# Optimization experiments

Measured on AMD Instinct MI355X. Metric: run time of the kernel, lower is better.

Reference implementation:

```python
import jax, jax.numpy as jnp
import numpy as np
import math

DILATION_RATES = (1, 2, 4, 8)


def setup_inputs() -> dict:
    key = jax.random.key(0)
    B, S, D = 2, 2048, 512
    R = len(DILATION_RATES)
    ks = jax.random.split(key, 8)
    s = 0.02  # init scale
    x = jax.random.normal(ks[0], (B, S, D), dtype=jnp.float32)
    Wq = jax.random.normal(ks[1], (D, D), dtype=jnp.float32) * s
    Wk = jax.random.normal(ks[2], (D, D), dtype=jnp.float32) * s
    Wv = jax.random.normal(ks[3], (D, D), dtype=jnp.float32) * s
    Wr = jax.random.normal(ks[4], (R, D, D), dtype=jnp.float32) * s  # per-rate projections
    Wo = jax.random.normal(ks[5], (R * D, D), dtype=jnp.float32) * s
    bq = jnp.zeros((D,), jnp.float32)
    bk = jnp.zeros((D,), jnp.float32)
    bv = jnp.zeros((D,), jnp.float32)
    br = jnp.zeros((R, D), jnp.float32)
    bo = jnp.zeros((D,), jnp.float32)
    return {"x": x, "Wq": Wq, "bq": bq, "Wk": Wk, "bk": bk, "Wv": Wv, "bv": bv,
            "Wr": Wr, "br": br, "Wo": Wo, "bo": bo}


def reference(x, Wq, bq, Wk, bk, Wv, bv, Wr, br, Wo, bo):
    B, S, D = x.shape
    Q = x @ Wq + bq
    K = x @ Wk + bk
    V = x @ Wv + bv
    # Dense scores are identical across rates in the original (recomputed each loop);
    # compute once for the same math.
    scores = jnp.einsum('bid,bjd->bij', Q, K) / math.sqrt(D)  # [B,S,S]
    idx = jnp.arange(S)
    outs, attns = [], []
    for r, rate in enumerate(DILATION_RATES):
        # mask[i, j] = 1 iff (j % rate == 0) and (j <= i)
        mask = (idx[None, :] % rate == 0) & (idx[None, :] <= idx[:, None])  # [S,S]
        sc = jnp.where(mask[None, :, :], scores, jnp.float32(-1e9))
        attn = jax.nn.softmax(sc, axis=-1)  # dropout is identity at eval
        attns.append(attn)
        ctx = jnp.einsum('bij,bjd->bid', attn, V)
        outs.append(ctx @ Wr[r] + br[r])
    combined = jnp.concatenate(outs, axis=-1)  # [B,S,4D]
    output = combined @ Wo + bo  # [B,S,D]
    avg_attention = jnp.mean(jnp.stack(attns, axis=0), axis=0)  # [B,S,S]
    return output, avg_attention
```

## Files before the change

### kernel.cpp

```cpp
#include <hip/hip_runtime.h>
#include <hip/hip_bf16.h>
#include <math.h>

#define B_ 2
#define S_ 2048
#define D_ 512
#define R_ 4
#define KP 3840

typedef __attribute__((ext_vector_type(8))) __bf16 bf16x8;
typedef __attribute__((ext_vector_type(4))) float f32x4;

enum { M_QKV = 0, M_SCORES = 1, M_WEFFT = 2, M_W2T = 3, M_PF = 4 };

__device__ __forceinline__ void g2l16(const void* gp, void* lp) {
    __builtin_amdgcn_global_load_lds(
        (const __attribute__((address_space(1))) unsigned int*)(unsigned long long)gp,
        (__attribute__((address_space(3))) unsigned int*)(unsigned int)(unsigned long long)lp,
        16, 0, 0);
}

template<int MODE, int TBM, int TBN>
__global__ __launch_bounds__(256) void mfma_nt(
    const short* __restrict__ A, const short* __restrict__ B,
    const float* __restrict__ bias, void* __restrict__ Cv,
    int lda, int ldb, int ldc, int K,
    long strA, long strB, long strC, long strBias, float scale)
{
    constexpr int WM = TBM / 2, WN = TBN / 2;
    constexpr int FM = WM / 16, FN = WN / 16;

    __shared__ __bf16 sAt[TBM * 64];
    __shared__ __bf16 sBt[TBN * 64];

    const int tid  = threadIdx.x;
    const int lane = tid & 63, wid = tid >> 6;
    const int ln15 = lane & 15, quad = lane >> 4;
    const int wy = wid & 1, wx = wid >> 1;

    const int by   = (MODE == M_PF) ? (gridDim.y - 1 - blockIdx.y) : blockIdx.y;
    const int col0 = blockIdx.x * TBN;
    const int row0 = by * TBM;
    const int z    = blockIdx.z;

    if constexpr (MODE == M_SCORES) {
        if (col0 > row0 + TBM - 1) return;
    }

    const short* Ab = A + (size_t)z * strA;
    const short* Bb = B + (size_t)z * strB;
    const float* biasb = bias + (size_t)z * strBias;

    int rate = 1, seg = 0;
    if constexpr (MODE == M_W2T) {
        int rIdx;
        if      (col0 >= 3584) { rate = 8; seg = 3584; rIdx = 3; }
        else if (col0 >= 3072) { rate = 4; seg = 3072; rIdx = 2; }
        else if (col0 >= 2048) { rate = 2; seg = 2048; rIdx = 1; }
        else                   { rate = 1; seg = 0;    rIdx = 0; }
        Ab += (size_t)rIdx * D_ * D_;
    }

    f32x4 acc[FM][FN];
    #pragma unroll
    for (int u = 0; u < FM; ++u)
        #pragma unroll
        for (int v = 0; v < FN; ++v)
            acc[u][v] = (f32x4){0.f, 0.f, 0.f, 0.f};

    for (int k0 = 0; k0 < K; k0 += 64) {
        if constexpr (MODE == M_PF) {
            int kr, ks;
            if      (k0 >= 3584) { kr = 8; ks = 3584; }
            else if (k0 >= 3072) { kr = 4; ks = 3072; }
            else if (k0 >= 2048) { kr = 2; ks = 2048; }
            else                 { kr = 1; ks = 0;    }
            if ((k0 - ks) * kr > row0 + TBM - 1) continue;
        }

        #pragma unroll
        for (int t = 0; t < TBM * 8; t += 256) {
            int idx = t + tid;
            int r = idx >> 3, c = idx & 7;
            const short* g = Ab + (size_t)(row0 + r) * lda + k0 + c * 8;
            g2l16(g, (char*)sAt + (t + wid * 64) * 16);
        }
        #pragma unroll
        for (int t = 0; t < TBN * 8; t += 256) {
            int idx = t + tid;
            int r = idx >> 3, c = idx & 7;
            int grow;
            if constexpr (MODE == M_W2T) grow = (col0 + r - seg) * rate;
            else                         grow = col0 + r;
            const short* g = Bb + (size_t)grow * ldb + k0 + c * 8;
            g2l16(g, (char*)sBt + (t + wid * 64) * 16);
        }
        __syncthreads();

        #pragma unroll
        for (int kk = 0; kk < 64; kk += 32) {
            bf16x8 af[FM], bfr[FN];
            #pragma unroll
            for (int u = 0; u < FM; ++u)
                af[u] = *(const bf16x8*)&sAt[(wy * WM + u * 16 + ln15) * 64 + kk + quad * 8];
            #pragma unroll
            for (int v = 0; v < FN; ++v)
                bfr[v] = *(const bf16x8*)&sBt[(wx * WN + v * 16 + ln15) * 64 + kk + quad * 8];
            #pragma unroll
            for (int u = 0; u < FM; ++u)
                #pragma unroll
                for (int v = 0; v < FN; ++v)
                    acc[u][v] = __builtin_amdgcn_mfma_f32_16x16x32_bf16(
                        af[u], bfr[v], acc[u][v], 0, 0, 0);
        }
        __syncthreads();
    }

    constexpr bool OUTBF = (MODE == M_QKV || MODE == M_WEFFT || MODE == M_W2T);
    #pragma unroll
    for (int u = 0; u < FM; ++u) {
        int rg = row0 + wy * WM + u * 16 + quad * 4;
        #pragma unroll
        for (int v = 0; v < FN; ++v) {
            int cg = col0 + wx * WN + v * 16 + ln15;
            float bv = 0.f;
            if constexpr (MODE == M_QKV || MODE == M_PF) bv = biasb[cg];
            #pragma unroll
            for (int rr = 0; rr < 4; ++rr) {
                float val = acc[u][v][rr];
                if constexpr (MODE == M_SCORES) val *= scale;
                val += bv;
                if constexpr (OUTBF)
                    ((__hip_bfloat16*)Cv)[(size_t)z * strC + (size_t)(rg + rr) * ldc + cg] =
                        __float2bfloat16(val);
                else
                    ((float*)Cv)[(size_t)z * strC + (size_t)(rg + rr) * ldc + cg] = val;
            }
        }
    }
}

__global__ __launch_bounds__(256) void cvt_bf16(const float* __restrict__ in,
                                                __hip_bfloat16* __restrict__ out, int n)
{
    int i = (blockIdx.x * 256 + threadIdx.x) * 4;
    if (i >= n) return;
    float4 v = *(const float4*)(in + i);
    out[i + 0] = __float2bfloat16(v.x);
    out[i + 1] = __float2bfloat16(v.y);
    out[i + 2] = __float2bfloat16(v.z);
    out[i + 3] = __float2bfloat16(v.w);
}

__global__ __launch_bounds__(256) void transpose3(const float* __restrict__ a,
                                                  const float* __restrict__ b,
                                                  const float* __restrict__ c,
                                                  __hip_bfloat16* __restrict__ out)
{
    const float* in = (blockIdx.z == 0) ? a : (blockIdx.z == 1) ? b : c;
    __hip_bfloat16* o = out + (size_t)blockIdx.z * 512 * 512;
    __shared__ float t[32][33];
    int c0 = blockIdx.x * 32, r0 = blockIdx.y * 32;
    int tx = threadIdx.x & 31, ty = threadIdx.x >> 5;
    #pragma unroll
    for (int dy = 0; dy < 32; dy += 8)
        t[ty + dy][tx] = in[(size_t)(r0 + ty + dy) * 512 + c0 + tx];
    __syncthreads();
    #pragma unroll
    for (int dy = 0; dy < 32; dy += 8)
        o[(size_t)(c0 + ty + dy) * 512 + r0 + tx] = __float2bfloat16(t[tx][ty + dy]);
}

__global__ __launch_bounds__(256) void transpose_cvt(const float* __restrict__ in,
                                                     __hip_bfloat16* __restrict__ out,
                                                     int Rr, int Cc)
{
    __shared__ float t[32][33];
    int c0 = blockIdx.x * 32, r0 = blockIdx.y * 32;
    int tx = threadIdx.x & 31, ty = threadIdx.x >> 5;
    #pragma unroll
    for (int dy = 0; dy < 32; dy += 8)
        t[ty + dy][tx] = in[(size_t)(r0 + ty + dy) * Cc + c0 + tx];
    __syncthreads();
    #pragma unroll
    for (int dy = 0; dy < 32; dy += 8)
        out[(size_t)(c0 + ty + dy) * Rr + r0 + tx] = __float2bfloat16(t[tx][ty + dy]);
}

__global__ __launch_bounds__(512) void prep_small(const float* __restrict__ bq,
                                                  const float* __restrict__ bk,
                                                  const float* __restrict__ bv,
                                                  const float* __restrict__ bo,
                                                  float* __restrict__ biasqkv,
                                                  float* __restrict__ beff)
{
    int t = threadIdx.x;
    biasqkv[t]        = bq[t];
    biasqkv[512 + t]  = bk[t];
    biasqkv[1024 + t] = bv[t];
    beff[t]           = bo[t];
}

__global__ __launch_bounds__(512) void beff_acc(const float* __restrict__ br,
                                                const float* __restrict__ Wo,
                                                float* __restrict__ beff)
{
    int n  = threadIdx.x;
    int m0 = blockIdx.x * 128;
    float acc = 0.f;
    #pragma unroll 4
    for (int m = m0; m < m0 + 128; ++m)
        acc += br[m] * Wo[(size_t)m * D_ + n];
    atomicAdd(&beff[n], acc);
}

__global__ __launch_bounds__(256) void softmax_p(const float* __restrict__ scores,
                                                 float* __restrict__ avg_out,
                                                 __hip_bfloat16* __restrict__ P)
{
    __shared__ float s_s[S_];
    __shared__ float s_p[S_];
    __shared__ float s_avg[S_];
    __shared__ float red[4];

    int i   = blockIdx.x;
    int b   = blockIdx.y;
    int tid = threadIdx.x;
    int wv  = tid >> 6;
    int ln  = tid & 63;

    const float* srow = scores + ((size_t)b * S_ + i) * S_;
    __hip_bfloat16* prow = P + ((size_t)b * S_ + i) * KP;

    for (int j = tid; j < S_; j += 256) s_avg[j] = 0.0f;
    for (int j = tid; j <= i; j += 256) s_s[j] = srow[j];
    __syncthreads();

    const int rates[4]  = {1, 2, 4, 8};
    const int segoff[4] = {0, 2048, 3072, 3584};
    const int imax = i | 63;

    for (int ri = 0; ri < 4; ++ri) {
        int rate   = rates[ri];
        int seg    = segoff[ri];
        int segLen = S_ / rate;
        int cnt    = i / rate + 1;
        int tlim   = min(segLen, ((imax / rate) & ~63) + 64);

        float m = -INFINITY;
        for (int t = tid; t < cnt; t += 256) m = fmaxf(m, s_s[t * rate]);
        #pragma unroll
        for (int o = 32; o > 0; o >>= 1) m = fmaxf(m, __shfl_down(m, o, 64));
        if (ln == 0) red[wv] = m;
        __syncthreads();
        m = fmaxf(fmaxf(red[0], red[1]), fmaxf(red[2], red[3]));
        __syncthreads();

        float sum = 0.0f;
        for (int t = tid; t < cnt; t += 256) {
            float e = __expf(s_s[t * rate] - m);
            s_p[t] = e;
            sum += e;
        }
        #pragma unroll
        for (int o = 32; o > 0; o >>= 1) sum += __shfl_down(sum, o, 64);
        if (ln == 0) red[wv] = sum;
        __syncthreads();
        sum = red[0] + red[1] + red[2] + red[3];
        float inv = 1.0f / sum;

        for (int t = tid; t < tlim; t += 256) {
            if (t < cnt) {
                float p = s_p[t] * inv;
                s_avg[t * rate] += 0.25f * p;
                prow[seg + t] = __float2bfloat16(p);
            } else {
                prow[seg + t] = __float2bfloat16(0.0f);
            }
        }
        __syncthreads();
    }

    float* arow = avg_out + ((size_t)b * S_ + i) * S_;
    for (int j = tid; j < S_; j += 256) arow[j] = s_avg[j];
}

extern "C" void kernel_launch(void* const* d_in, const int* in_sizes, int n_in,
                              void* d_out, int out_size, void* d_ws, size_t ws_size,
                              hipStream_t stream)
{
    const float* x  = (const float*)d_in[0];
    const float* Wq = (const float*)d_in[1];
    const float* bq = (const float*)d_in[2];
    const float* Wk = (const float*)d_in[3];
    const float* bk = (const float*)d_in[4];
    const float* Wv = (const float*)d_in[5];
    const float* bv = (const float*)d_in[6];
    const float* Wr = (const float*)d_in[7];
    const float* br = (const float*)d_in[8];
    const float* Wo = (const float*)d_in[9];
    const float* bo = (const float*)d_in[10];

    float* out    = (float*)d_out;
    float* scores = out + (size_t)B_ * S_ * D_;

    char* wsb = (char*)d_ws;
    short* xb  = (short*)(wsb);
    short* Qb  = (short*)(wsb + (4u << 20));
    short* Kb  = (short*)(wsb + (8u << 20));
    short* Vb  = (short*)(wsb + (12u << 20));
    short* P   = (short*)(wsb + (16u << 20));
    short* W2T = (short*)(wsb + (16u << 20) + 31457280u);
    float* beff    = (float*)(wsb + (16u << 20) + 31457280u + 7864320u);
    float* biasqkv = beff + 512;
    short* WqT   = P;
    short* Wrb   = (short*)((char*)P + 1572864);
    short* WoT   = (short*)((char*)P + 3670016);
    short* WeffT = (short*)((char*)P + 5767168);

    const float scale = (float)(1.0 / sqrt((double)D_));

    prep_small<<<1, 512, 0, stream>>>(bq, bk, bv, bo, biasqkv, beff);
    beff_acc<<<16, 512, 0, stream>>>(br, Wo, beff);
    cvt_bf16<<<dim3(2048), 256, 0, stream>>>(x,  (__hip_bfloat16*)xb,  B_ * S_ * D_);
    cvt_bf16<<<dim3(1024), 256, 0, stream>>>(Wr, (__hip_bfloat16*)Wrb, R_ * D_ * D_);
    transpose3<<<dim3(16, 16, 3), 256, 0, stream>>>(Wq, Wk, Wv, (__hip_bfloat16*)WqT);
    transpose_cvt<<<dim3(16, 64), 256, 0, stream>>>(Wo, (__hip_bfloat16*)WoT, 2048, 512);

    mfma_nt<M_QKV, 64, 128><<<dim3(4, 64, 3), 256, 0, stream>>>(
        xb, WqT, biasqkv, Qb, 512, 512, 512, 512,
        0, 512L * 512, (long)B_ * S_ * D_, 512, 0.f);

    mfma_nt<M_SCORES, 64, 128><<<dim3(16, 32, 2), 256, 0, stream>>>(
        Qb, Kb, beff, scores, 512, 512, 2048, 512,
        (long)S_ * D_, (long)S_ * D_, (long)S_ * S_, 0, scale);

    mfma_nt<M_WEFFT, 64, 64><<<dim3(8, 8, 4), 256, 0, stream>>>(
        WoT, Wrb, beff, WeffT, 2048, 512, 512, 512,
        512, (long)D_ * D_, (long)D_ * D_, 0, 0.f);

    mfma_nt<M_W2T, 64, 128><<<dim3(30, 8, 2), 256, 0, stream>>>(
        WeffT, Vb, beff, W2T, 512, 512, 3840, 512,
        0, (long)S_ * D_, 512L * KP, 0, 0.f);

    softmax_p<<<dim3(S_, B_), 256, 0, stream>>>(scores, scores, (__hip_bfloat16*)P);

    mfma_nt<M_PF, 64, 64><<<dim3(8, 32, 2), 256, 0, stream>>>(
        P, W2T, beff, out, 3840, 3840, 512, 3840,
        (long)S_ * KP, 512L * KP, (long)S_ * D_, 0, 0.f);
}
```

Baseline: 242.2 us.

## Use swizzled 128-wide K tiles, single-pass multi-rate softmax, and fused prep kernels

The GEMM K-tile is doubled to 128 and the LDS layout gets an XOR swizzle, which halves the barrier count per tile and reduces bank conflicts on fragment reads. The softmax kernel now computes a single exp pass over the causal row and derives each rate's normalizer from eight strided partial sums, replacing four separate max/sum passes. It also writes P with vectorized bf16x8 stores and computes the average attention directly. The prep conversion and transpose kernels are merged into two launches. Using one shared max across all rates changes the numerics slightly, and the softmax now pads P to 128-wide segments. The larger LDS footprint may lower GEMM occupancy.

```diff
diff --git a/kernel.cpp b/kernel.cpp
--- a/kernel.cpp
+++ b/kernel.cpp
@@ -30,8 +30,8 @@
     constexpr int WM = TBM / 2, WN = TBN / 2;
     constexpr int FM = WM / 16, FN = WN / 16;
 
-    __shared__ __bf16 sAt[TBM * 64];
-    __shared__ __bf16 sBt[TBN * 64];
+    __shared__ __bf16 sAt[TBM * 128];
+    __shared__ __bf16 sBt[TBN * 128];
 
     const int tid  = threadIdx.x;
     const int lane = tid & 63, wid = tid >> 6;
@@ -68,7 +68,7 @@
         for (int v = 0; v < FN; ++v)
             acc[u][v] = (f32x4){0.f, 0.f, 0.f, 0.f};
 
-    for (int k0 = 0; k0 < K; k0 += 64) {
+    for (int k0 = 0; k0 < K; k0 += 128) {
         if constexpr (MODE == M_PF) {
             int kr, ks;
             if      (k0 >= 3584) { kr = 8; ks = 3584; }
@@ -79,33 +79,39 @@
         }
 
         #pragma unroll
-        for (int t = 0; t < TBM * 8; t += 256) {
+        for (int t = 0; t < TBM * 16; t += 256) {
             int idx = t + tid;
-            int r = idx >> 3, c = idx & 7;
-            const short* g = Ab + (size_t)(row0 + r) * lda + k0 + c * 8;
+            int r = idx >> 4, clog = (idx & 15) ^ (r & 7);
+            const short* g = Ab + (size_t)(row0 + r) * lda + k0 + clog * 8;
             g2l16(g, (char*)sAt + (t + wid * 64) * 16);
         }
         #pragma unroll
-        for (int t = 0; t < TBN * 8; t += 256) {
+        for (int t = 0; t < TBN * 16; t += 256) {
             int idx = t + tid;
-            int r = idx >> 3, c = idx & 7;
+            int r = idx >> 4, clog = (idx & 15) ^ (r & 7);
             int grow;
             if constexpr (MODE == M_W2T) grow = (col0 + r - seg) * rate;
             else                         grow = col0 + r;
-            const short* g = Bb + (size_t)grow * ldb + k0 + c * 8;
+            const short* g = Bb + (size_t)grow * ldb + k0 + clog * 8;
             g2l16(g, (char*)sBt + (t + wid * 64) * 16);
         }
         __syncthreads();
 
         #pragma unroll
-        for (int kk = 0; kk < 64; kk += 32) {
+        for (int kk = 0; kk < 128; kk += 32) {
             bf16x8 af[FM], bfr[FN];
             #pragma unroll
-            for (int u = 0; u < FM; ++u)
-                af[u] = *(const bf16x8*)&sAt[(wy * WM + u * 16 + ln15) * 64 + kk + quad * 8];
-            #pragma unroll
-            for (int v = 0; v < FN; ++v)
-                bfr[v] = *(const bf16x8*)&sBt[(wx * WN + v * 16 + ln15) * 64 + kk + quad * 8];
+            for (int u = 0; u < FM; ++u) {
+                int ra = wy * WM + u * 16 + ln15;
+                int ch = (kk >> 3) + quad;
+                af[u] = *(const bf16x8*)&sAt[ra * 128 + (ch ^ (ra & 7)) * 8];
+            }
+            #pragma unroll
+            for (int v = 0; v < FN; ++v) {
+                int rb = wx * WN + v * 16 + ln15;
+                int ch = (kk >> 3) + quad;
+                bfr[v] = *(const bf16x8*)&sBt[rb * 128 + (ch ^ (rb & 7)) * 8];
+            }
             #pragma unroll
             for (int u = 0; u < FM; ++u)
                 #pragma unroll
@@ -140,47 +146,46 @@
     }
 }
 
-__global__ __launch_bounds__(256) void cvt_bf16(const float* __restrict__ in,
-                                                __hip_bfloat16* __restrict__ out, int n)
-{
-    int i = (blockIdx.x * 256 + threadIdx.x) * 4;
-    if (i >= n) return;
-    float4 v = *(const float4*)(in + i);
-    out[i + 0] = __float2bfloat16(v.x);
-    out[i + 1] = __float2bfloat16(v.y);
-    out[i + 2] = __float2bfloat16(v.z);
-    out[i + 3] = __float2bfloat16(v.w);
-}
-
-__global__ __launch_bounds__(256) void transpose3(const float* __restrict__ a,
-                                                  const float* __restrict__ b,
-                                                  const float* __restrict__ c,
-                                                  __hip_bfloat16* __restrict__ out)
-{
-    const float* in = (blockIdx.z == 0) ? a : (blockIdx.z == 1) ? b : c;
-    __hip_bfloat16* o = out + (size_t)blockIdx.z * 512 * 512;
+__global__ __launch_bounds__(256) void prep_cvt(const float* __restrict__ x,
+                                                const float* __restrict__ Wr,
+                                                __hip_bfloat16* __restrict__ xb,
+                                                __hip_bfloat16* __restrict__ Wrb)
+{
+    const size_t NX = (size_t)B_ * S_ * D_;
+    size_t i = ((size_t)blockIdx.x * 256 + threadIdx.x) * 4;
+    const float* in; __hip_bfloat16* out; size_t off;
+    if (i < NX) { in = x; out = xb; off = i; }
+    else        { in = Wr; out = Wrb; off = i - NX; }
+    float4 v = *(const float4*)(in + off);
+    out[off + 0] = __float2bfloat16(v.x);
+    out[off + 1] = __float2bfloat16(v.y);
+    out[off + 2] = __float2bfloat16(v.z);
+    out[off + 3] = __float2bfloat16(v.w);
+}
+
+__global__ __launch_bounds__(256) void prep_transpose(const float* __restrict__ Wq,
+                                                      const float* __restrict__ Wk,
+                                                      const float* __restrict__ Wv,
+                                                      const float* __restrict__ Wo,
+                                                      __hip_bfloat16* __restrict__ WqT,
+                                                      __hip_bfloat16* __restrict__ WoT)
+{
     __shared__ float t[32][33];
-    int c0 = blockIdx.x * 32, r0 = blockIdx.y * 32;
+    int y = blockIdx.y;
+    const float* in; __hip_bfloat16* out; int Rr, r0;
+    if (y < 48) {
+        int w = y >> 4;
+        in = (w == 0) ? Wq : (w == 1) ? Wk : Wv;
+        out = WqT + (size_t)w * 512 * 512;
+        Rr = 512; r0 = (y & 15) * 32;
+    } else {
+        in = Wo; out = WoT; Rr = 2048; r0 = (y - 48) * 32;
+    }
+    int c0 = blockIdx.x * 32;
     int tx = threadIdx.x & 31, ty = threadIdx.x >> 5;
     #pragma unroll
     for (int dy = 0; dy < 32; dy += 8)
         t[ty + dy][tx] = in[(size_t)(r0 + ty + dy) * 512 + c0 + tx];
-    __syncthreads();
-    #pragma unroll
-    for (int dy = 0; dy < 32; dy += 8)
-        o[(size_t)(c0 + ty + dy) * 512 + r0 + tx] = __float2bfloat16(t[tx][ty + dy]);
-}
-
-__global__ __launch_bounds__(256) void transpose_cvt(const float* __restrict__ in,
-                                                     __hip_bfloat16* __restrict__ out,
-                                                     int Rr, int Cc)
-{
-    __shared__ float t[32][33];
-    int c0 = blockIdx.x * 32, r0 = blockIdx.y * 32;
-    int tx = threadIdx.x & 31, ty = threadIdx.x >> 5;
-    #pragma unroll
-    for (int dy = 0; dy < 32; dy += 8)
-        t[ty + dy][tx] = in[(size_t)(r0 + ty + dy) * Cc + c0 + tx];
     __syncthreads();
     #pragma unroll
     for (int dy = 0; dy < 32; dy += 8)
@@ -218,10 +223,9 @@
                                                  float* __restrict__ avg_out,
                                                  __hip_bfloat16* __restrict__ P)
 {
-    __shared__ float s_s[S_];
     __shared__ float s_p[S_];
-    __shared__ float s_avg[S_];
     __shared__ float red[4];
+    __shared__ float bs[8];
 
     int i   = blockIdx.x;
     int b   = blockIdx.y;
@@ -230,59 +234,103 @@
     int ln  = tid & 63;
 
     const float* srow = scores + ((size_t)b * S_ + i) * S_;
-    __hip_bfloat16* prow = P + ((size_t)b * S_ + i) * KP;
-
-    for (int j = tid; j < S_; j += 256) s_avg[j] = 0.0f;
-    for (int j = tid; j <= i; j += 256) s_s[j] = srow[j];
+    __bf16* prow = (__bf16*)(P + ((size_t)b * S_ + i) * KP);
+
+    const int cnt1 = i + 1;
+    const int n4   = cnt1 >> 2;
+
+    float m = -INFINITY;
+    for (int t = tid; t < n4; t += 256) {
+        float4 v = ((const float4*)srow)[t];
+        ((float4*)s_p)[t] = v;
+        m = fmaxf(m, fmaxf(fmaxf(v.x, v.y), fmaxf(v.z, v.w)));
+    }
+    for (int j = (n4 << 2) + tid; j < cnt1; j += 256) {
+        float v = srow[j]; s_p[j] = v; m = fmaxf(m, v);
+    }
+    #pragma unroll
+    for (int o = 32; o > 0; o >>= 1) m = fmaxf(m, __shfl_xor(m, o, 64));
+    if (ln == 0) red[wv] = m;
+    if (tid < 8) bs[tid] = 0.f;
     __syncthreads();
-
-    const int rates[4]  = {1, 2, 4, 8};
-    const int segoff[4] = {0, 2048, 3072, 3584};
-    const int imax = i | 63;
-
+    m = fmaxf(fmaxf(red[0], red[1]), fmaxf(red[2], red[3]));
+
+    float a0 = 0.f, a1 = 0.f, a2 = 0.f, a3 = 0.f;
+    for (int t = tid; t < n4; t += 256) {
+        float4 v = ((float4*)s_p)[t];
+        v.x = __expf(v.x - m); v.y = __expf(v.y - m);
+        v.z = __expf(v.z - m); v.w = __expf(v.w - m);
+        ((float4*)s_p)[t] = v;
+        a0 += v.x; a1 += v.y; a2 += v.z; a3 += v.w;
+    }
+    for (int j = (n4 << 2) + tid; j < cnt1; j += 256) {
+        float e = __expf(s_p[j] - m); s_p[j] = e;
+        atomicAdd(&bs[j & 7], e);
+    }
+    float o0 = __shfl_xor(a0, 1, 64), o1 = __shfl_xor(a1, 1, 64);
+    float o2 = __shfl_xor(a2, 1, 64), o3 = __shfl_xor(a3, 1, 64);
+    float b8[8];
+    if ((ln & 1) == 0) {
+        b8[0]=a0; b8[1]=a1; b8[2]=a2; b8[3]=a3; b8[4]=o0; b8[5]=o1; b8[6]=o2; b8[7]=o3;
+    } else {
+        b8[0]=o0; b8[1]=o1; b8[2]=o2; b8[3]=o3; b8[4]=a0; b8[5]=a1; b8[6]=a2; b8[7]=a3;
+    }
+    #pragma unroll
+    for (int st = 2; st < 64; st <<= 1)
+        #pragma unroll
+        for (int k = 0; k < 8; ++k) b8[k] += __shfl_xor(b8[k], st, 64);
+    if (ln == 0) {
+        #pragma unroll
+        for (int k = 0; k < 8; ++k) atomicAdd(&bs[k], b8[k]);
+    }
+    __syncthreads();
+
+    float S1 = bs[0]+bs[1]+bs[2]+bs[3]+bs[4]+bs[5]+bs[6]+bs[7];
+    float S2 = bs[0]+bs[2]+bs[4]+bs[6];
+    float S4 = bs[0]+bs[4];
+    float S8 = bs[0];
+    float i1 = 1.f/S1, i2 = 1.f/S2, i4 = 1.f/S4, i8 = 1.f/S8;
+    float c0 = 0.25f*(i1+i2+i4+i8), c1 = 0.25f*i1, c2 = 0.25f*(i1+i2);
+    float c4 = 0.25f*(i1+i2+i4);
+    float cA[4] = {c0, c1, c2, c1};
+    float cB[4] = {c4, c1, c2, c1};
+
+    float* arow = avg_out + ((size_t)b * S_ + i) * S_;
+    for (int t = tid; t < S_ / 4; t += 256) {
+        int j = t << 2;
+        float4 e = ((float4*)s_p)[t];
+        const float* cc = (t & 1) ? cB : cA;
+        float4 o;
+        o.x = (j     < cnt1) ? e.x * cc[0] : 0.f;
+        o.y = (j + 1 < cnt1) ? e.y * cc[1] : 0.f;
+        o.z = (j + 2 < cnt1) ? e.z * cc[2] : 0.f;
+        o.w = (j + 3 < cnt1) ? e.w * cc[3] : 0.f;
+        ((float4*)arow)[t] = o;
+    }
+
+    const float invSr[4] = {i1, i2, i4, i8};
+    const int   segoff[4] = {0, 2048, 3072, 3584};
+    const int   imax = i | 63;
+    #pragma unroll
     for (int ri = 0; ri < 4; ++ri) {
-        int rate   = rates[ri];
         int seg    = segoff[ri];
-        int segLen = S_ / rate;
-        int cnt    = i / rate + 1;
-        int tlim   = min(segLen, ((imax / rate) & ~63) + 64);
-
-        float m = -INFINITY;
-        for (int t = tid; t < cnt; t += 256) m = fmaxf(m, s_s[t * rate]);
-        #pragma unroll
-        for (int o = 32; o > 0; o >>= 1) m = fmaxf(m, __shfl_down(m, o, 64));
-        if (ln == 0) red[wv] = m;
-        __syncthreads();
-        m = fmaxf(fmaxf(red[0], red[1]), fmaxf(red[2], red[3]));
-        __syncthreads();
-
-        float sum = 0.0f;
-        for (int t = tid; t < cnt; t += 256) {
-            float e = __expf(s_s[t * rate] - m);
-            s_p[t] = e;
-            sum += e;
-        }
-        #pragma unroll
-        for (int o = 32; o > 0; o >>= 1) sum += __shfl_down(sum, o, 64);
-        if (ln == 0) red[wv] = sum;
-        __syncthreads();
-        sum = red[0] + red[1] + red[2] + red[3];
-        float inv = 1.0f / sum;
-
-        for (int t = tid; t < tlim; t += 256) {
-            if (t < cnt) {
-                float p = s_p[t] * inv;
-                s_avg[t * rate] += 0.25f * p;
-                prow[seg + t] = __float2bfloat16(p);
-            } else {
-                prow[seg + t] = __float2bfloat16(0.0f);
+        int segLen = S_ >> ri;
+        int cnt    = (i >> ri) + 1;
+        int tlim   = min(segLen, ((imax >> ri) & ~127) + 128);
+        float invS = invSr[ri];
+        int nch = tlim >> 3;
+        for (int t8 = tid; t8 < nch; t8 += 256) {
+            int t0 = t8 << 3;
+            bf16x8 w;
+            #pragma unroll
+            for (int k = 0; k < 8; ++k) {
+                int t = t0 + k;
+                float p = (t < cnt) ? s_p[t << ri] * invS : 0.f;
+                w[k] = (__bf16)p;
             }
-        }
-        __syncthreads();
-    }
-
-    float* arow = avg_out + ((size_t)b * S_ + i) * S_;
-    for (int j = tid; j < S_; j += 256) arow[j] = s_avg[j];
+            *((bf16x8*)(prow + seg) + t8) = w;
+        }
+    }
 }
 
 extern "C" void kernel_launch(void* const* d_in, const int* in_sizes, int n_in,
@@ -322,10 +370,10 @@
 
     prep_small<<<1, 512, 0, stream>>>(bq, bk, bv, bo, biasqkv, beff);
     beff_acc<<<16, 512, 0, stream>>>(br, Wo, beff);
-    cvt_bf16<<<dim3(2048), 256, 0, stream>>>(x,  (__hip_bfloat16*)xb,  B_ * S_ * D_);
-    cvt_bf16<<<dim3(1024), 256, 0, stream>>>(Wr, (__hip_bfloat16*)Wrb, R_ * D_ * D_);
-    transpose3<<<dim3(16, 16, 3), 256, 0, stream>>>(Wq, Wk, Wv, (__hip_bfloat16*)WqT);
-    transpose_cvt<<<dim3(16, 64), 256, 0, stream>>>(Wo, (__hip_bfloat16*)WoT, 2048, 512);
+    prep_cvt<<<dim3(3072), 256, 0, stream>>>(x, Wr, (__hip_bfloat16*)xb,
+                                             (__hip_bfloat16*)Wrb);
+    prep_transpose<<<dim3(16, 112), 256, 0, stream>>>(
+        Wq, Wk, Wv, Wo, (__hip_bfloat16*)WqT, (__hip_bfloat16*)WoT);
 
     mfma_nt<M_QKV, 64, 128><<<dim3(4, 64, 3), 256, 0, stream>>>(
         xb, WqT, biasqkv, Qb, 512, 512, 512, 512,
```

New measurement: 207.4 us. -14.4%, faster.
